# Kernel optimization log

Measured on AMD Instinct MI355X. Metric: run time of the kernel, lower is better.

## Reference

```python
import jax, jax.numpy as jnp
import numpy as np

EPS = 1e-10      # normalizer eps from the torch module
IN_EPS = 1e-5    # torch InstanceNorm2d default eps
STRIDE = 2
PAD = 1


def _dw_conv_transpose(x, W):
    """Depthwise ConvTranspose2d applied for every output channel at once.

    x: [B, Cin, H, W]
    W: [Cin, Cout, kh, kw]  (W[:, i] is sub_convs[i].weight of shape [Cin, 1, kh, kw])
    returns: [B, Cin, Cout, H', W'] where channel (c, i) = convT of x[:, c] with W[c, i].
    """
    Cin, Cout, kh, kw = W.shape
    # Transposed conv == dilated conv with spatially flipped kernel,
    # lhs_dilation = stride, padding = k - 1 - pad (output_padding = 0).
    rhs = jnp.flip(W, axis=(-2, -1)).reshape(Cin * Cout, 1, kh, kw)
    pad_h = (kh - 1 - PAD, kh - 1 - PAD)
    pad_w = (kw - 1 - PAD, kw - 1 - PAD)
    out = jax.lax.conv_general_dilated(
        x, rhs,
        window_strides=(1, 1),
        padding=(pad_h, pad_w),
        lhs_dilation=(STRIDE, STRIDE),
        dimension_numbers=('NCHW', 'OIHW', 'NCHW'),
        feature_group_count=Cin,
    )  # [B, Cin*Cout, H', W'], group-major: group c -> channels c*Cout:(c+1)*Cout
    B = x.shape[0]
    return out.reshape(B, Cin, Cout, out.shape[2], out.shape[3])


def setup_inputs() -> dict:
    key = jax.random.key(0)
    k1, k2, k3 = jax.random.split(key, 3)
    B, Cin, Cout, H, Wd, K = 2, 64, 64, 48, 48, 4
    x = jax.random.normal(k1, (B, Cin, H, Wd), dtype=jnp.float32)
    # Positive-leaning weights keep the normalizer (convT of ones) away from zero.
    W = 0.05 + 0.1 * jax.random.uniform(k2, (Cin, Cout, K, K), dtype=jnp.float32)
    bias = 0.02 * jax.random.normal(k3, (Cout,), dtype=jnp.float32)
    return {"x": x, "W": W, "bias": bias}


def reference(x, W, bias):
    # numerator: depthwise convT of the input for every (in_ch, out_ch) pair
    num = _dw_conv_transpose(x, W)                       # [B, Cin, Cout, H', W']
    # normalizer: same convT applied to ones (batch-independent -> batch of 1)
    den = _dw_conv_transpose(jnp.ones_like(x[:1]), W) + EPS  # [1, Cin, Cout, H', W']
    out = jnp.sum(num / den, axis=1) + bias[None, :, None, None]  # [B, Cout, H', W']
    # InstanceNorm2d (no affine, biased variance) over spatial dims per (b, c)
    mean = jnp.mean(out, axis=(2, 3), keepdims=True)
    var = jnp.var(out, axis=(2, 3), keepdims=True)
    return (out - mean) / jnp.sqrt(var + IN_EPS)
```

## Files before the change

### kernel.cpp

```cpp
#include <hip/hip_runtime.h>

#define BB    2
#define CIN   64
#define NI    64
#define HIN   48
#define WIN   48
#define HO    96
#define WO    96
#define EPSN  1e-10f
#define IN_EPS 1e-5f
#define IMG   (HO*WO)
#define NIMG  (BB*NI)
#define LPH   50
#define LPW   56
#define LPAD  4

template <int CS>
__global__ __launch_bounds__(256, 2) void conv_kernel(
        const float* __restrict__ x, const float* __restrict__ Wt,
        float* __restrict__ part) {
    constexpr int NC = CIN / CS;
    const int bi = blockIdx.x, s = blockIdx.y;
    const int b = bi >> 6, i = bi & 63, c0 = s * NC;
    const int tid = threadIdx.x;
    const int ty = tid >> 4, tx = tid & 15;

    __shared__ __align__(16) float sX[2][LPH * LPW];
    __shared__ __align__(16) float sF[NC * 16];
    __shared__ float sW[NC * 16];
    __shared__ float sR[NC * 16];
    __shared__ float sFix[384];

    {
        const float4 z = make_float4(0.f, 0.f, 0.f, 0.f);
        float4* p0 = (float4*)&sX[0][0];
        for (int e = tid; e < 2 * LPH * LPW / 4; e += 256) p0[e] = z;
    }
    for (int e = tid; e < NC * 16; e += 256) {
        const int c = e >> 4, j = e & 15;
        const float* wp = Wt + ((size_t)(c0 + c) * NI + i) * 16;
        sW[e] = wp[j];
        const int py = (j >> 3) & 1, px = (j >> 2) & 1, a = (j >> 1) & 1, bb = j & 1;
        const int kh = py ? (a ? 2 : 0) : (a ? 3 : 1);
        const int kw = px ? (bb ? 2 : 0) : (bb ? 3 : 1);
        const int r0 = py ? 0 : 1, r1 = py ? 2 : 3;
        const int q0 = px ? 0 : 1, q1 = px ? 2 : 3;
        const float den = wp[r0 * 4 + q0] + wp[r0 * 4 + q1]
                        + wp[r1 * 4 + q0] + wp[r1 * 4 + q1];
        sF[e] = wp[kh * 4 + kw] / (den + EPSN);
        const int cy = j >> 2, cx = j & 3;
        const int THn[4] = {1, 2, 2, 1};
        const int THv[4][2] = {{1, 1}, {0, 2}, {1, 3}, {2, 2}};
        float den2 = 0.f;
        for (int aa = 0; aa < THn[cy]; ++aa)
            for (int bb2 = 0; bb2 < THn[cx]; ++bb2)
                den2 += wp[THv[cy][aa] * 4 + THv[cx][bb2]];
        sR[e] = 1.f / (den2 + EPSN);
    }

    int ldsOff[3];
#pragma unroll
    for (int k = 0; k < 3; ++k) {
        const int e = tid + 256 * k;
        const int h = e / 12, w4 = e - 12 * h;
        ldsOff[k] = (h + 1) * LPW + LPAD + 4 * w4;
    }
    const float4* xg = (const float4*)x + (size_t)(b * CIN + c0) * 576;

    int q0A0, q0A1, q0B0, q0B1, w00, w01, w02, w03, cls0;
    int q1A0, q1A1, q1B0, q1B1, w10, w11, w12, w13, cls1;
#pragma unroll
    for (int k = 0; k < 2; ++k) {
        const int p = tid + 256 * k;
        if (k == 1 && p >= 380) break;
        int y, xo;
        if (p < 96)       { y = 0;            xo = p; }
        else if (p < 192) { y = 95;           xo = p - 96; }
        else if (p < 286) { y = p - 192 + 1;  xo = 0; }
        else              { y = p - 286 + 1;  xo = 95; }
        const int hA = (y + 1) >> 1, hB = hA - 1;
        const int khA = (y & 1) ? 0 : 1, khB = khA + 2;
        const int wA = (xo + 1) >> 1, wB = wA - 1;
        const int kwA = (xo & 1) ? 0 : 1, kwB = kwA + 2;
        const int cy = (y == 0) ? 0 : (y == 95) ? 3 : ((y & 1) ? 1 : 2);
        const int cx = (xo == 0) ? 0 : (xo == 95) ? 3 : ((xo & 1) ? 1 : 2);
        const int rA = (hA + 1) * LPW, rB = (hB + 1) * LPW;
        if (k == 0) {
            q0A0 = rA + LPAD + wA; q0A1 = rA + LPAD + wB;
            q0B0 = rB + LPAD + wA; q0B1 = rB + LPAD + wB;
            w00 = khA * 4 + kwA; w01 = khA * 4 + kwB;
            w02 = khB * 4 + kwA; w03 = khB * 4 + kwB;
            cls0 = cy * 4 + cx;
        } else {
            q1A0 = rA + LPAD + wA; q1A1 = rA + LPAD + wB;
            q1B0 = rB + LPAD + wA; q1B1 = rB + LPAD + wB;
            w10 = khA * 4 + kwA; w11 = khA * 4 + kwB;
            w12 = khB * 4 + kwA; w13 = khB * 4 + kwB;
            cls1 = cy * 4 + cx;
        }
    }

    __syncthreads();

    {
        float4 a0 = xg[tid], a1 = xg[tid + 256], a2;
        if (tid < 64) a2 = xg[tid + 512];
        float* dst = &sX[0][0];
        *(float4*)(dst + ldsOff[0]) = a0;
        *(float4*)(dst + ldsOff[1]) = a1;
        if (tid < 64) *(float4*)(dst + ldsOff[2]) = a2;
    }
    __syncthreads();

    float acc[6][6];
#pragma unroll
    for (int r = 0; r < 6; ++r)
#pragma unroll
        for (int j = 0; j < 6; ++j) acc[r][j] = 0.f;
    float fixAcc0 = 0.f, fixAcc1 = 0.f;

    const int patchBase = (3 * ty) * LPW + 3 * tx + (LPAD - 1);

#pragma unroll 2
    for (int c = 0; c < NC; ++c) {
        float4 a0, a1, a2;
        if (c + 1 < NC) {
            const float4* xn = xg + (size_t)(c + 1) * 576;
            a0 = xn[tid]; a1 = xn[tid + 256];
            if (tid < 64) a2 = xn[tid + 512];
        }

        const float* __restrict__ xs = &sX[c & 1][0];

        float g[16];
        {
            const float4* gf = (const float4*)&sF[c * 16];
#pragma unroll
            for (int q = 0; q < 4; ++q) {
                const float4 t = gf[q];
                g[4 * q] = t.x; g[4 * q + 1] = t.y;
                g[4 * q + 2] = t.z; g[4 * q + 3] = t.w;
            }
        }

        float xv[5][5];
#pragma unroll
        for (int rr = 0; rr < 5; ++rr)
#pragma unroll
            for (int cc = 0; cc < 5; ++cc)
                xv[rr][cc] = xs[patchBase + rr * LPW + cc];

#pragma unroll
        for (int r = 0; r < 6; ++r) {
            const int rhi = (r + 3) >> 1, rlo = rhi - 1, py = r & 1;
#pragma unroll
            for (int j = 0; j < 6; ++j) {
                const int chi = (j + 3) >> 1, clo = chi - 1, px = j & 1;
                const float* gg = &g[py * 8 + px * 4];
                acc[r][j] += xv[rhi][chi] * gg[0] + xv[rhi][clo] * gg[1]
                           + xv[rlo][chi] * gg[2] + xv[rlo][clo] * gg[3];
            }
        }

        {
            const float* wc = &sW[c * 16];
            const float num0 = xs[q0A0] * wc[w00] + xs[q0A1] * wc[w01]
                             + xs[q0B0] * wc[w02] + xs[q0B1] * wc[w03];
            fixAcc0 += num0 * sR[c * 16 + cls0];
            if (tid < 124) {
                const float num1 = xs[q1A0] * wc[w10] + xs[q1A1] * wc[w11]
                                 + xs[q1B0] * wc[w12] + xs[q1B1] * wc[w13];
                fixAcc1 += num1 * sR[c * 16 + cls1];
            }
        }

        if (c + 1 < NC) {
            float* dst = &sX[(c + 1) & 1][0];
            *(float4*)(dst + ldsOff[0]) = a0;
            *(float4*)(dst + ldsOff[1]) = a1;
            if (tid < 64) *(float4*)(dst + ldsOff[2]) = a2;
        }
        __syncthreads();
    }

    sFix[tid] = fixAcc0;
    if (tid < 124) sFix[tid + 256] = fixAcc1;
    __syncthreads();

#pragma unroll
    for (int r = 0; r < 6; ++r)
#pragma unroll
        for (int j = 0; j < 6; ++j) {
            const int y = 6 * ty + r, xo = 6 * tx + j;
            if (y == 0)        acc[r][j] = sFix[xo];
            else if (y == 95)  acc[r][j] = sFix[96 + xo];
            else if (xo == 0)  acc[r][j] = sFix[192 + y - 1];
            else if (xo == 95) acc[r][j] = sFix[286 + y - 1];
        }

    float* pp = part + ((size_t)s * NIMG + bi) * IMG + (6 * ty) * WO + 6 * tx;
#pragma unroll
    for (int r = 0; r < 6; ++r)
#pragma unroll
        for (int jj = 0; jj < 3; ++jj) {
            float2 v;
            v.x = acc[r][2 * jj];
            v.y = acc[r][2 * jj + 1];
            *(float2*)(pp + r * WO + 2 * jj) = v;
        }
}

template <int CS>
__global__ __launch_bounds__(768) void epilogue_kernel(
        const float* __restrict__ part, const float* __restrict__ bias,
        float* __restrict__ out) {
    const int bi = blockIdx.x;
    const int tid = threadIdx.x;
    const float bv = bias[bi & 63];
    const float4* pb = (const float4*)part + (size_t)bi * (IMG / 4);
    const size_t stride4 = (size_t)NIMG * (IMG / 4);

    float4 v[3];
    float s1 = 0.f, s2 = 0.f;
#pragma unroll
    for (int k = 0; k < 3; ++k) {
        const int idx = k * 768 + tid;
        float4 t = pb[idx];
#pragma unroll
        for (int s = 1; s < CS; ++s) {
            const float4 q = pb[s * stride4 + idx];
            t.x += q.x; t.y += q.y; t.z += q.z; t.w += q.w;
        }
        t.x += bv; t.y += bv; t.z += bv; t.w += bv;
        v[k] = t;
        s1 += t.x + t.y + t.z + t.w;
        s2 += t.x * t.x + t.y * t.y + t.z * t.z + t.w * t.w;
    }

    __shared__ float red[24];
    __shared__ float stat[2];
#pragma unroll
    for (int off = 32; off > 0; off >>= 1) {
        s1 += __shfl_down(s1, off, 64);
        s2 += __shfl_down(s2, off, 64);
    }
    const int w = tid >> 6;
    if ((tid & 63) == 0) { red[w] = s1; red[12 + w] = s2; }
    __syncthreads();
    if (tid == 0) {
        float t1 = 0.f, t2 = 0.f;
#pragma unroll
        for (int k = 0; k < 12; ++k) { t1 += red[k]; t2 += red[12 + k]; }
        const float mean = t1 * (1.f / 9216.f);
        const float m2 = t2 * (1.f / 9216.f);
        stat[0] = mean;
        stat[1] = rsqrtf(m2 - mean * mean + IN_EPS);
    }
    __syncthreads();
    const float mean = stat[0], inv = stat[1];

    float4* ob = (float4*)out + (size_t)bi * (IMG / 4);
#pragma unroll
    for (int k = 0; k < 3; ++k) {
        const int idx = k * 768 + tid;
        float4 t = v[k];
        t.x = (t.x - mean) * inv; t.y = (t.y - mean) * inv;
        t.z = (t.z - mean) * inv; t.w = (t.w - mean) * inv;
        ob[idx] = t;
    }
}

extern "C" void kernel_launch(void* const* d_in, const int* in_sizes, int n_in,
                              void* d_out, int out_size, void* d_ws, size_t ws_size,
                              hipStream_t stream) {
    const float* x    = (const float*)d_in[0];
    const float* Wt   = (const float*)d_in[1];
    const float* bias = (const float*)d_in[2];
    float* out = (float*)d_out;
    float* ws  = (float*)d_ws;

    const size_t need4 = (size_t)4 * NIMG * IMG * 4;
    if (ws_size >= need4) {
        conv_kernel<4><<<dim3(NIMG, 4), 256, 0, stream>>>(x, Wt, ws);
        epilogue_kernel<4><<<NIMG, 768, 0, stream>>>(ws, bias, out);
    } else {
        conv_kernel<1><<<dim3(NIMG, 1), 256, 0, stream>>>(x, Wt, out);
        epilogue_kernel<1><<<NIMG, 768, 0, stream>>>(out, bias, out);
    }
}
```

Before: 89.88 us.

## Precompute weight ratios in prep kernel and retile conv to 192 threads, 6x8 outputs

Adds a prep kernel that computes the per-(out,in) normalized filter taps and boundary reciprocals once, and has the conv kernel read them from global memory instead of recomputing them in every block. The conv kernel is retiled to 192 threads, each producing a 6x8 output patch that loads its input patch with a float4 plus two edge scalars, using a tighter 52-wide shared tile. The bias add moves from the epilogue into the conv store, and the stores widen to float4. This removes redundant divisions and cuts LDS loads per output, at the cost of an extra kernel launch, fewer threads per block, and higher register pressure.

```diff
diff --git a/kernel.cpp b/kernel.cpp
--- a/kernel.cpp
+++ b/kernel.cpp
@@ -11,67 +11,96 @@
 #define IN_EPS 1e-5f
 #define IMG   (HO*WO)
 #define NIMG  (BB*NI)
-#define LPH   50
-#define LPW   56
-#define LPAD  4
-
-template <int CS>
-__global__ __launch_bounds__(256, 2) void conv_kernel(
-        const float* __restrict__ x, const float* __restrict__ Wt,
-        float* __restrict__ part) {
-    constexpr int NC = CIN / CS;
-    const int bi = blockIdx.x, s = blockIdx.y;
-    const int b = bi >> 6, i = bi & 63, c0 = s * NC;
-    const int tid = threadIdx.x;
-    const int ty = tid >> 4, tx = tid & 15;
-
-    __shared__ __align__(16) float sX[2][LPH * LPW];
-    __shared__ __align__(16) float sF[NC * 16];
-    __shared__ float sW[NC * 16];
-    __shared__ float sR[NC * 16];
-    __shared__ float sFix[384];
-
-    {
-        const float4 z = make_float4(0.f, 0.f, 0.f, 0.f);
-        float4* p0 = (float4*)&sX[0][0];
-        for (int e = tid; e < 2 * LPH * LPW / 4; e += 256) p0[e] = z;
-    }
-    for (int e = tid; e < NC * 16; e += 256) {
-        const int c = e >> 4, j = e & 15;
-        const float* wp = Wt + ((size_t)(c0 + c) * NI + i) * 16;
-        sW[e] = wp[j];
+
+#define TW    52
+#define TROWS 50
+#define TILE  (TROWS*TW)
+
+__device__ float g_F[NI * CIN * 16];
+__device__ float g_R[NI * CIN * 16];
+
+__global__ __launch_bounds__(256) void prep_kernel(const float* __restrict__ Wt) {
+    const int e = blockIdx.x * 256 + threadIdx.x;
+    const int i = e >> 6, c = e & 63;
+    float w[16];
+    const float* wp = Wt + ((size_t)c * NI + i) * 16;
+#pragma unroll
+    for (int j = 0; j < 16; ++j) w[j] = wp[j];
+    float* F = g_F + (size_t)e * 16;
+    float* R = g_R + (size_t)e * 16;
+#pragma unroll
+    for (int j = 0; j < 16; ++j) {
         const int py = (j >> 3) & 1, px = (j >> 2) & 1, a = (j >> 1) & 1, bb = j & 1;
         const int kh = py ? (a ? 2 : 0) : (a ? 3 : 1);
         const int kw = px ? (bb ? 2 : 0) : (bb ? 3 : 1);
         const int r0 = py ? 0 : 1, r1 = py ? 2 : 3;
         const int q0 = px ? 0 : 1, q1 = px ? 2 : 3;
-        const float den = wp[r0 * 4 + q0] + wp[r0 * 4 + q1]
-                        + wp[r1 * 4 + q0] + wp[r1 * 4 + q1];
-        sF[e] = wp[kh * 4 + kw] / (den + EPSN);
+        const float den = w[r0 * 4 + q0] + w[r0 * 4 + q1]
+                        + w[r1 * 4 + q0] + w[r1 * 4 + q1];
+        F[j] = w[kh * 4 + kw] / (den + EPSN);
         const int cy = j >> 2, cx = j & 3;
         const int THn[4] = {1, 2, 2, 1};
         const int THv[4][2] = {{1, 1}, {0, 2}, {1, 3}, {2, 2}};
         float den2 = 0.f;
         for (int aa = 0; aa < THn[cy]; ++aa)
             for (int bb2 = 0; bb2 < THn[cx]; ++bb2)
-                den2 += wp[THv[cy][aa] * 4 + THv[cx][bb2]];
-        sR[e] = 1.f / (den2 + EPSN);
+                den2 += w[THv[cy][aa] * 4 + THv[cx][bb2]];
+        R[j] = 1.f / (den2 + EPSN);
+    }
+}
+
+template <int CS>
+__global__ __launch_bounds__(192, 2) void conv_kernel(
+        const float* __restrict__ x, const float* __restrict__ Wt,
+        const float* __restrict__ bias, float* __restrict__ part) {
+    constexpr int NC = CIN / CS;
+    const int bi = blockIdx.x, s = blockIdx.y;
+    const int b = bi >> 6, i = bi & 63, c0 = s * NC;
+    const int tid = threadIdx.x;
+    const int ty = tid / 12, tx = tid - 12 * ty;
+
+    __shared__ __align__(16) float sX[2][TILE];
+    __shared__ float sW[NC * 16];
+    __shared__ float sR[NC * 16];
+    __shared__ float sFix[384];
+
+    {
+        const float4 z = make_float4(0.f, 0.f, 0.f, 0.f);
+        for (int e = tid; e < 2 * TROWS; e += 192) {
+            const int q = e / TROWS, row = e - q * TROWS;
+            float* rp = &sX[q][row * TW];
+            if (row == 0 || row == TROWS - 1) {
+#pragma unroll
+                for (int k = 0; k < TW; k += 4) *(float4*)(rp + k) = z;
+            } else {
+                *(float4*)(rp + 48) = z;
+            }
+        }
+    }
+    for (int e = tid; e < NC * 16; e += 192) {
+        const int c = e >> 4, j = e & 15;
+        sW[e] = Wt[((size_t)(c0 + c) * NI + i) * 16 + j];
+        sR[e] = g_R[((size_t)(i * CIN) + c0 + c) * 16 + j];
     }
 
     int ldsOff[3];
 #pragma unroll
     for (int k = 0; k < 3; ++k) {
-        const int e = tid + 256 * k;
-        const int h = e / 12, w4 = e - 12 * h;
-        ldsOff[k] = (h + 1) * LPW + LPAD + 4 * w4;
+        const int e = tid + 192 * k;
+        const int row = e / 12, c4 = e - 12 * row;
+        ldsOff[k] = (row + 1) * TW + 4 * c4;
     }
     const float4* xg = (const float4*)x + (size_t)(b * CIN + c0) * 576;
 
-    int q0A0, q0A1, q0B0, q0B1, w00, w01, w02, w03, cls0;
-    int q1A0, q1A1, q1B0, q1B1, w10, w11, w12, w13, cls1;
+    const int rowBase = 3 * ty;
+    const int cMain = 4 * tx;
+    const int cE0 = (tx == 0) ? 48 : 4 * tx - 1;
+    const int cE5 = (tx == 11) ? 48 : 4 * tx + 4;
+
+    int qA0[2], qA1[2], qB0[2], qB1[2], wI[2][4], clsI[2];
 #pragma unroll
     for (int k = 0; k < 2; ++k) {
-        const int p = tid + 256 * k;
+        const int p = tid + 192 * k;
         if (k == 1 && p >= 380) break;
         int y, xo;
         if (p < 96)       { y = 0;            xo = p; }
@@ -82,141 +111,134 @@
         const int khA = (y & 1) ? 0 : 1, khB = khA + 2;
         const int wA = (xo + 1) >> 1, wB = wA - 1;
         const int kwA = (xo & 1) ? 0 : 1, kwB = kwA + 2;
+        const int colA = wA;
+        const int colB = (wB < 0) ? 48 : wB;
+        const int rA = (hA + 1) * TW, rB = (hB + 1) * TW;
+        qA0[k] = rA + colA; qA1[k] = rA + colB;
+        qB0[k] = rB + colA; qB1[k] = rB + colB;
+        wI[k][0] = khA * 4 + kwA; wI[k][1] = khA * 4 + kwB;
+        wI[k][2] = khB * 4 + kwA; wI[k][3] = khB * 4 + kwB;
         const int cy = (y == 0) ? 0 : (y == 95) ? 3 : ((y & 1) ? 1 : 2);
         const int cx = (xo == 0) ? 0 : (xo == 95) ? 3 : ((xo & 1) ? 1 : 2);
-        const int rA = (hA + 1) * LPW, rB = (hB + 1) * LPW;
-        if (k == 0) {
-            q0A0 = rA + LPAD + wA; q0A1 = rA + LPAD + wB;
-            q0B0 = rB + LPAD + wA; q0B1 = rB + LPAD + wB;
-            w00 = khA * 4 + kwA; w01 = khA * 4 + kwB;
-            w02 = khB * 4 + kwA; w03 = khB * 4 + kwB;
-            cls0 = cy * 4 + cx;
-        } else {
-            q1A0 = rA + LPAD + wA; q1A1 = rA + LPAD + wB;
-            q1B0 = rB + LPAD + wA; q1B1 = rB + LPAD + wB;
-            w10 = khA * 4 + kwA; w11 = khA * 4 + kwB;
-            w12 = khB * 4 + kwA; w13 = khB * 4 + kwB;
-            cls1 = cy * 4 + cx;
-        }
-    }
-
+        clsI[k] = cy * 4 + cx;
+    }
+
+    {
+        const float4 a0 = xg[tid], a1 = xg[tid + 192], a2 = xg[tid + 384];
+        float* d = &sX[0][0];
+        *(float4*)(d + ldsOff[0]) = a0;
+        *(float4*)(d + ldsOff[1]) = a1;
+        *(float4*)(d + ldsOff[2]) = a2;
+    }
     __syncthreads();
 
-    {
-        float4 a0 = xg[tid], a1 = xg[tid + 256], a2;
-        if (tid < 64) a2 = xg[tid + 512];
-        float* dst = &sX[0][0];
-        *(float4*)(dst + ldsOff[0]) = a0;
-        *(float4*)(dst + ldsOff[1]) = a1;
-        if (tid < 64) *(float4*)(dst + ldsOff[2]) = a2;
-    }
-    __syncthreads();
-
-    float acc[6][6];
+    float acc[6][8];
 #pragma unroll
     for (int r = 0; r < 6; ++r)
 #pragma unroll
-        for (int j = 0; j < 6; ++j) acc[r][j] = 0.f;
+        for (int j = 0; j < 8; ++j) acc[r][j] = 0.f;
     float fixAcc0 = 0.f, fixAcc1 = 0.f;
 
-    const int patchBase = (3 * ty) * LPW + 3 * tx + (LPAD - 1);
+    const float* Fg = g_F + ((size_t)(i * CIN) + c0) * 16;
 
 #pragma unroll 2
     for (int c = 0; c < NC; ++c) {
         float4 a0, a1, a2;
         if (c + 1 < NC) {
             const float4* xn = xg + (size_t)(c + 1) * 576;
-            a0 = xn[tid]; a1 = xn[tid + 256];
-            if (tid < 64) a2 = xn[tid + 512];
-        }
-
-        const float* __restrict__ xs = &sX[c & 1][0];
+            a0 = xn[tid]; a1 = xn[tid + 192]; a2 = xn[tid + 384];
+        }
 
         float g[16];
         {
-            const float4* gf = (const float4*)&sF[c * 16];
-#pragma unroll
-            for (int q = 0; q < 4; ++q) {
-                const float4 t = gf[q];
-                g[4 * q] = t.x; g[4 * q + 1] = t.y;
-                g[4 * q + 2] = t.z; g[4 * q + 3] = t.w;
-            }
-        }
-
-        float xv[5][5];
-#pragma unroll
-        for (int rr = 0; rr < 5; ++rr)
-#pragma unroll
-            for (int cc = 0; cc < 5; ++cc)
-                xv[rr][cc] = xs[patchBase + rr * LPW + cc];
+            const float* fp = Fg + c * 16;
+#pragma unroll
+            for (int k = 0; k < 16; ++k) g[k] = fp[k];
+        }
+
+        const float* __restrict__ xs = &sX[c & 1][0];
+
+        float xv[5][6];
+#pragma unroll
+        for (int pr = 0; pr < 5; ++pr) {
+            const int ro = (rowBase + pr) * TW;
+            xv[pr][0] = xs[ro + cE0];
+            const float4 m = *(const float4*)(xs + ro + cMain);
+            xv[pr][1] = m.x; xv[pr][2] = m.y; xv[pr][3] = m.z; xv[pr][4] = m.w;
+            xv[pr][5] = xs[ro + cE5];
+        }
 
 #pragma unroll
         for (int r = 0; r < 6; ++r) {
-            const int rhi = (r + 3) >> 1, rlo = rhi - 1, py = r & 1;
-#pragma unroll
-            for (int j = 0; j < 6; ++j) {
-                const int chi = (j + 3) >> 1, clo = chi - 1, px = j & 1;
+            const int prA = ((r + 1) >> 1) + 1, prB = prA - 1;
+            const int py = r & 1;
+#pragma unroll
+            for (int j = 0; j < 8; ++j) {
+                const int pcA = ((j + 1) >> 1) + 1, pcB = pcA - 1;
+                const int px = j & 1;
                 const float* gg = &g[py * 8 + px * 4];
-                acc[r][j] += xv[rhi][chi] * gg[0] + xv[rhi][clo] * gg[1]
-                           + xv[rlo][chi] * gg[2] + xv[rlo][clo] * gg[3];
+                acc[r][j] += xv[prA][pcA] * gg[0] + xv[prA][pcB] * gg[1]
+                           + xv[prB][pcA] * gg[2] + xv[prB][pcB] * gg[3];
             }
         }
 
         {
             const float* wc = &sW[c * 16];
-            const float num0 = xs[q0A0] * wc[w00] + xs[q0A1] * wc[w01]
-                             + xs[q0B0] * wc[w02] + xs[q0B1] * wc[w03];
-            fixAcc0 += num0 * sR[c * 16 + cls0];
-            if (tid < 124) {
-                const float num1 = xs[q1A0] * wc[w10] + xs[q1A1] * wc[w11]
-                                 + xs[q1B0] * wc[w12] + xs[q1B1] * wc[w13];
-                fixAcc1 += num1 * sR[c * 16 + cls1];
+            const float num0 = xs[qA0[0]] * wc[wI[0][0]] + xs[qA1[0]] * wc[wI[0][1]]
+                             + xs[qB0[0]] * wc[wI[0][2]] + xs[qB1[0]] * wc[wI[0][3]];
+            fixAcc0 += num0 * sR[c * 16 + clsI[0]];
+            if (tid < 188) {
+                const float num1 = xs[qA0[1]] * wc[wI[1][0]] + xs[qA1[1]] * wc[wI[1][1]]
+                                 + xs[qB0[1]] * wc[wI[1][2]] + xs[qB1[1]] * wc[wI[1][3]];
+                fixAcc1 += num1 * sR[c * 16 + clsI[1]];
             }
         }
 
         if (c + 1 < NC) {
-            float* dst = &sX[(c + 1) & 1][0];
-            *(float4*)(dst + ldsOff[0]) = a0;
-            *(float4*)(dst + ldsOff[1]) = a1;
-            if (tid < 64) *(float4*)(dst + ldsOff[2]) = a2;
+            float* d = &sX[(c + 1) & 1][0];
+            *(float4*)(d + ldsOff[0]) = a0;
+            *(float4*)(d + ldsOff[1]) = a1;
+            *(float4*)(d + ldsOff[2]) = a2;
         }
         __syncthreads();
     }
 
     sFix[tid] = fixAcc0;
-    if (tid < 124) sFix[tid + 256] = fixAcc1;
+    if (tid < 188) sFix[192 + tid] = fixAcc1;
     __syncthreads();
 
 #pragma unroll
     for (int r = 0; r < 6; ++r)
 #pragma unroll
-        for (int j = 0; j < 6; ++j) {
-            const int y = 6 * ty + r, xo = 6 * tx + j;
+        for (int j = 0; j < 8; ++j) {
+            const int y = 6 * ty + r, xo = 8 * tx + j;
             if (y == 0)        acc[r][j] = sFix[xo];
             else if (y == 95)  acc[r][j] = sFix[96 + xo];
             else if (xo == 0)  acc[r][j] = sFix[192 + y - 1];
             else if (xo == 95) acc[r][j] = sFix[286 + y - 1];
         }
 
-    float* pp = part + ((size_t)s * NIMG + bi) * IMG + (6 * ty) * WO + 6 * tx;
-#pragma unroll
-    for (int r = 0; r < 6; ++r)
-#pragma unroll
-        for (int jj = 0; jj < 3; ++jj) {
-            float2 v;
-            v.x = acc[r][2 * jj];
-            v.y = acc[r][2 * jj + 1];
-            *(float2*)(pp + r * WO + 2 * jj) = v;
-        }
+    const float bvq = bias[i] * (1.f / CS);
+    float* pp = part + ((size_t)s * NIMG + bi) * IMG + (6 * ty) * WO + 8 * tx;
+#pragma unroll
+    for (int r = 0; r < 6; ++r) {
+#pragma unroll
+        for (int h = 0; h < 2; ++h) {
+            float4 v;
+            v.x = acc[r][4 * h]     + bvq;
+            v.y = acc[r][4 * h + 1] + bvq;
+            v.z = acc[r][4 * h + 2] + bvq;
+            v.w = acc[r][4 * h + 3] + bvq;
+            *(float4*)(pp + r * WO + 4 * h) = v;
+        }
+    }
 }
 
 template <int CS>
 __global__ __launch_bounds__(768) void epilogue_kernel(
-        const float* __restrict__ part, const float* __restrict__ bias,
-        float* __restrict__ out) {
+        const float* __restrict__ part, float* __restrict__ out) {
     const int bi = blockIdx.x;
     const int tid = threadIdx.x;
-    const float bv = bias[bi & 63];
     const float4* pb = (const float4*)part + (size_t)bi * (IMG / 4);
     const size_t stride4 = (size_t)NIMG * (IMG / 4);
 
@@ -231,7 +253,6 @@
             const float4 q = pb[s * stride4 + idx];
             t.x += q.x; t.y += q.y; t.z += q.z; t.w += q.w;
         }
-        t.x += bv; t.y += bv; t.z += bv; t.w += bv;
         v[k] = t;
         s1 += t.x + t.y + t.z + t.w;
         s2 += t.x * t.x + t.y * t.y + t.z * t.z + t.w * t.w;
@@ -279,12 +300,14 @@
     float* out = (float*)d_out;
     float* ws  = (float*)d_ws;
 
+    prep_kernel<<<16, 256, 0, stream>>>(Wt);
+
     const size_t need4 = (size_t)4 * NIMG * IMG * 4;
     if (ws_size >= need4) {
-        conv_kernel<4><<<dim3(NIMG, 4), 256, 0, stream>>>(x, Wt, ws);
-        epilogue_kernel<4><<<NIMG, 768, 0, stream>>>(ws, bias, out);
+        conv_kernel<4><<<dim3(NIMG, 4), 192, 0, stream>>>(x, Wt, bias, ws);
+        epilogue_kernel<4><<<NIMG, 768, 0, stream>>>(ws, out);
     } else {
-        conv_kernel<1><<<dim3(NIMG, 1), 256, 0, stream>>>(x, Wt, out);
-        epilogue_kernel<1><<<NIMG, 768, 0, stream>>>(out, bias, out);
+        conv_kernel<1><<<dim3(NIMG, 1), 192, 0, stream>>>(x, Wt, bias, out);
+        epilogue_kernel<1><<<NIMG, 768, 0, stream>>>(out, out);
     }
 }
```

Measured after the change: 94.73 us. 5.4% more time.

## Fuse conv and instance-norm epilogue via last-block atomic counter

Applied to the files above, without the earlier changes.

Merges the conv kernel and the epilogue into one launch. Each channel-split block writes its partial image to a global device buffer, then bumps a per-image atomic counter, and the last-arriving block sums the partials and applies bias plus instance norm. This removes a kernel launch and the gap between the two kernels. In exchange the final reduction runs on only 128 blocks of 256 threads, each holding 9 float4 values per thread, which raises register pressure. The counter is reset inside the kernel for the next call.

```diff
diff --git a/kernel.cpp b/kernel.cpp
--- a/kernel.cpp
+++ b/kernel.cpp
@@ -11,30 +11,37 @@
 #define IN_EPS 1e-5f
 #define IMG   (HO*WO)
 #define NIMG  (BB*NI)
+#define CS    4
+#define NC    (CIN/CS)
+
 #define LPH   50
 #define LPW   56
 #define LPAD  4
-
-template <int CS>
-__global__ __launch_bounds__(256, 2) void conv_kernel(
+#define TILE  (LPH*LPW)
+
+__device__ float g_part[CS * NIMG * IMG];
+__device__ int   g_cnt[NIMG];
+
+__global__ __launch_bounds__(256, 2) void fused_kernel(
         const float* __restrict__ x, const float* __restrict__ Wt,
-        float* __restrict__ part) {
-    constexpr int NC = CIN / CS;
+        const float* __restrict__ bias, float* __restrict__ out) {
     const int bi = blockIdx.x, s = blockIdx.y;
     const int b = bi >> 6, i = bi & 63, c0 = s * NC;
     const int tid = threadIdx.x;
     const int ty = tid >> 4, tx = tid & 15;
 
-    __shared__ __align__(16) float sX[2][LPH * LPW];
+    __shared__ __align__(16) float sX[2][TILE];
     __shared__ __align__(16) float sF[NC * 16];
     __shared__ float sW[NC * 16];
     __shared__ float sR[NC * 16];
     __shared__ float sFix[384];
+    __shared__ float sRed[26];
+    __shared__ int   sOld;
 
     {
         const float4 z = make_float4(0.f, 0.f, 0.f, 0.f);
         float4* p0 = (float4*)&sX[0][0];
-        for (int e = tid; e < 2 * LPH * LPW / 4; e += 256) p0[e] = z;
+        for (int e = tid; e < 2 * TILE / 4; e += 256) p0[e] = z;
     }
     for (int e = tid; e < NC * 16; e += 256) {
         const int c = e >> 4, j = e & 15;
@@ -62,13 +69,12 @@
 #pragma unroll
     for (int k = 0; k < 3; ++k) {
         const int e = tid + 256 * k;
-        const int h = e / 12, w4 = e - 12 * h;
-        ldsOff[k] = (h + 1) * LPW + LPAD + 4 * w4;
+        const int row = e / 12, w4 = e - 12 * row;
+        ldsOff[k] = (row + 1) * LPW + LPAD + 4 * w4;
     }
     const float4* xg = (const float4*)x + (size_t)(b * CIN + c0) * 576;
 
-    int q0A0, q0A1, q0B0, q0B1, w00, w01, w02, w03, cls0;
-    int q1A0, q1A1, q1B0, q1B1, w10, w11, w12, w13, cls1;
+    int qA0[2], qA1[2], qB0[2], qB1[2], wI[2][4], clsI[2];
 #pragma unroll
     for (int k = 0; k < 2; ++k) {
         const int p = tid + 256 * k;
@@ -82,22 +88,14 @@
         const int khA = (y & 1) ? 0 : 1, khB = khA + 2;
         const int wA = (xo + 1) >> 1, wB = wA - 1;
         const int kwA = (xo & 1) ? 0 : 1, kwB = kwA + 2;
+        const int rA = (hA + 1) * LPW, rB = (hB + 1) * LPW;
+        qA0[k] = rA + LPAD + wA; qA1[k] = rA + LPAD + wB;
+        qB0[k] = rB + LPAD + wA; qB1[k] = rB + LPAD + wB;
+        wI[k][0] = khA * 4 + kwA; wI[k][1] = khA * 4 + kwB;
+        wI[k][2] = khB * 4 + kwA; wI[k][3] = khB * 4 + kwB;
         const int cy = (y == 0) ? 0 : (y == 95) ? 3 : ((y & 1) ? 1 : 2);
         const int cx = (xo == 0) ? 0 : (xo == 95) ? 3 : ((xo & 1) ? 1 : 2);
-        const int rA = (hA + 1) * LPW, rB = (hB + 1) * LPW;
-        if (k == 0) {
-            q0A0 = rA + LPAD + wA; q0A1 = rA + LPAD + wB;
-            q0B0 = rB + LPAD + wA; q0B1 = rB + LPAD + wB;
-            w00 = khA * 4 + kwA; w01 = khA * 4 + kwB;
-            w02 = khB * 4 + kwA; w03 = khB * 4 + kwB;
-            cls0 = cy * 4 + cx;
-        } else {
-            q1A0 = rA + LPAD + wA; q1A1 = rA + LPAD + wB;
-            q1B0 = rB + LPAD + wA; q1B1 = rB + LPAD + wB;
-            w10 = khA * 4 + kwA; w11 = khA * 4 + kwB;
-            w12 = khB * 4 + kwA; w13 = khB * 4 + kwB;
-            cls1 = cy * 4 + cx;
-        }
+        clsI[k] = cy * 4 + cx;
     }
 
     __syncthreads();
@@ -105,10 +103,10 @@
     {
         float4 a0 = xg[tid], a1 = xg[tid + 256], a2;
         if (tid < 64) a2 = xg[tid + 512];
-        float* dst = &sX[0][0];
-        *(float4*)(dst + ldsOff[0]) = a0;
-        *(float4*)(dst + ldsOff[1]) = a1;
-        if (tid < 64) *(float4*)(dst + ldsOff[2]) = a2;
+        float* d = &sX[0][0];
+        *(float4*)(d + ldsOff[0]) = a0;
+        *(float4*)(d + ldsOff[1]) = a1;
+        if (tid < 64) *(float4*)(d + ldsOff[2]) = a2;
     }
     __syncthreads();
 
@@ -164,21 +162,21 @@
 
         {
             const float* wc = &sW[c * 16];
-            const float num0 = xs[q0A0] * wc[w00] + xs[q0A1] * wc[w01]
-                             + xs[q0B0] * wc[w02] + xs[q0B1] * wc[w03];
-            fixAcc0 += num0 * sR[c * 16 + cls0];
+            const float num0 = xs[qA0[0]] * wc[wI[0][0]] + xs[qA1[0]] * wc[wI[0][1]]
+                             + xs[qB0[0]] * wc[wI[0][2]] + xs[qB1[0]] * wc[wI[0][3]];
+            fixAcc0 += num0 * sR[c * 16 + clsI[0]];
             if (tid < 124) {
-                const float num1 = xs[q1A0] * wc[w10] + xs[q1A1] * wc[w11]
-                                 + xs[q1B0] * wc[w12] + xs[q1B1] * wc[w13];
-                fixAcc1 += num1 * sR[c * 16 + cls1];
+                const float num1 = xs[qA0[1]] * wc[wI[1][0]] + xs[qA1[1]] * wc[wI[1][1]]
+                                 + xs[qB0[1]] * wc[wI[1][2]] + xs[qB1[1]] * wc[wI[1][3]];
+                fixAcc1 += num1 * sR[c * 16 + clsI[1]];
             }
         }
 
         if (c + 1 < NC) {
-            float* dst = &sX[(c + 1) & 1][0];
-            *(float4*)(dst + ldsOff[0]) = a0;
-            *(float4*)(dst + ldsOff[1]) = a1;
-            if (tid < 64) *(float4*)(dst + ldsOff[2]) = a2;
+            float* d = &sX[(c + 1) & 1][0];
+            *(float4*)(d + ldsOff[0]) = a0;
+            *(float4*)(d + ldsOff[1]) = a1;
+            if (tid < 64) *(float4*)(d + ldsOff[2]) = a2;
         }
         __syncthreads();
     }
@@ -198,37 +196,37 @@
             else if (xo == 95) acc[r][j] = sFix[286 + y - 1];
         }
 
-    float* pp = part + ((size_t)s * NIMG + bi) * IMG + (6 * ty) * WO + 6 * tx;
-#pragma unroll
-    for (int r = 0; r < 6; ++r)
-#pragma unroll
-        for (int jj = 0; jj < 3; ++jj) {
-            float2 v;
-            v.x = acc[r][2 * jj];
-            v.y = acc[r][2 * jj + 1];
-            *(float2*)(pp + r * WO + 2 * jj) = v;
-        }
-}
-
-template <int CS>
-__global__ __launch_bounds__(768) void epilogue_kernel(
-        const float* __restrict__ part, const float* __restrict__ bias,
-        float* __restrict__ out) {
-    const int bi = blockIdx.x;
-    const int tid = threadIdx.x;
-    const float bv = bias[bi & 63];
-    const float4* pb = (const float4*)part + (size_t)bi * (IMG / 4);
-    const size_t stride4 = (size_t)NIMG * (IMG / 4);
-
-    float4 v[3];
+    {
+        float* pp = g_part + ((size_t)s * NIMG + bi) * IMG + (6 * ty) * WO + 6 * tx;
+#pragma unroll
+        for (int r = 0; r < 6; ++r)
+#pragma unroll
+            for (int jj = 0; jj < 3; ++jj) {
+                float2 v;
+                v.x = acc[r][2 * jj];
+                v.y = acc[r][2 * jj + 1];
+                *(float2*)(pp + r * WO + 2 * jj) = v;
+            }
+    }
+
+    __threadfence();
+    __syncthreads();
+    if (tid == 0) sOld = atomicAdd(&g_cnt[bi], 1);
+    __syncthreads();
+    if (sOld != CS - 1) return;
+    __threadfence();
+
+    const float bv = bias[i];
+    const float4* pb = (const float4*)g_part;
+    float4 v[9];
     float s1 = 0.f, s2 = 0.f;
 #pragma unroll
-    for (int k = 0; k < 3; ++k) {
-        const int idx = k * 768 + tid;
-        float4 t = pb[idx];
-#pragma unroll
-        for (int s = 1; s < CS; ++s) {
-            const float4 q = pb[s * stride4 + idx];
+    for (int k = 0; k < 9; ++k) {
+        const int pix4 = k * 256 + tid;
+        float4 t = pb[(size_t)bi * 2304 + pix4];
+#pragma unroll
+        for (int sp = 1; sp < CS; ++sp) {
+            const float4 q = pb[((size_t)sp * NIMG + bi) * 2304 + pix4];
             t.x += q.x; t.y += q.y; t.z += q.z; t.w += q.w;
         }
         t.x += bv; t.y += bv; t.z += bv; t.w += bv;
@@ -237,36 +235,34 @@
         s2 += t.x * t.x + t.y * t.y + t.z * t.z + t.w * t.w;
     }
 
-    __shared__ float red[24];
-    __shared__ float stat[2];
 #pragma unroll
     for (int off = 32; off > 0; off >>= 1) {
         s1 += __shfl_down(s1, off, 64);
         s2 += __shfl_down(s2, off, 64);
     }
     const int w = tid >> 6;
-    if ((tid & 63) == 0) { red[w] = s1; red[12 + w] = s2; }
+    if ((tid & 63) == 0) { sRed[w] = s1; sRed[4 + w] = s2; }
     __syncthreads();
     if (tid == 0) {
-        float t1 = 0.f, t2 = 0.f;
-#pragma unroll
-        for (int k = 0; k < 12; ++k) { t1 += red[k]; t2 += red[12 + k]; }
+        const float t1 = sRed[0] + sRed[1] + sRed[2] + sRed[3];
+        const float t2 = sRed[4] + sRed[5] + sRed[6] + sRed[7];
         const float mean = t1 * (1.f / 9216.f);
         const float m2 = t2 * (1.f / 9216.f);
-        stat[0] = mean;
-        stat[1] = rsqrtf(m2 - mean * mean + IN_EPS);
-    }
-    __syncthreads();
-    const float mean = stat[0], inv = stat[1];
-
-    float4* ob = (float4*)out + (size_t)bi * (IMG / 4);
-#pragma unroll
-    for (int k = 0; k < 3; ++k) {
-        const int idx = k * 768 + tid;
+        sRed[24] = mean;
+        sRed[25] = rsqrtf(m2 - mean * mean + IN_EPS);
+        g_cnt[bi] = 0;
+    }
+    __syncthreads();
+    const float mean = sRed[24], inv = sRed[25];
+
+    float4* ob = (float4*)out + (size_t)bi * 2304;
+#pragma unroll
+    for (int k = 0; k < 9; ++k) {
+        const int pix4 = k * 256 + tid;
         float4 t = v[k];
         t.x = (t.x - mean) * inv; t.y = (t.y - mean) * inv;
         t.z = (t.z - mean) * inv; t.w = (t.w - mean) * inv;
-        ob[idx] = t;
+        ob[pix4] = t;
     }
 }
 
@@ -277,14 +273,7 @@
     const float* Wt   = (const float*)d_in[1];
     const float* bias = (const float*)d_in[2];
     float* out = (float*)d_out;
-    float* ws  = (float*)d_ws;
-
-    const size_t need4 = (size_t)4 * NIMG * IMG * 4;
-    if (ws_size >= need4) {
-        conv_kernel<4><<<dim3(NIMG, 4), 256, 0, stream>>>(x, Wt, ws);
-        epilogue_kernel<4><<<NIMG, 768, 0, stream>>>(ws, bias, out);
-    } else {
-        conv_kernel<1><<<dim3(NIMG, 1), 256, 0, stream>>>(x, Wt, out);
-        epilogue_kernel<1><<<NIMG, 768, 0, stream>>>(out, bias, out);
-    }
+    (void)d_ws; (void)ws_size;
+
+    fused_kernel<<<dim3(NIMG, CS), 256, 0, stream>>>(x, Wt, bias, out);
 }
```

New measurement: 166.9 us. +85.7%, slower.
